# Kernel tuning notes

Hardware: AMD Instinct MI355X
Metric: run time of the kernel (lower is better)

The kernel has to match this reference:

```python
import jax, jax.numpy as jnp
import numpy as np

D = 256; H = 4; DK = D // H
MAX_ATOMS = 13; EDGE_NUM = 78; PAD = 799; K = 20
PREFIX = MAX_ATOMS * 2 + 2 + EDGE_NUM * 4   # 340, tokens that get positional encoding
SEQ = PREFIX + K                             # 360
NPAIR = EDGE_NUM + MAX_ATOMS                 # 91 atom pairs (i,j), j up to max_atoms
DFF = 2048; MSP = 800; B = 256

# ---- static pair / gather index tables (numpy, computed once) ----
def _pairs():
    pi, pj, pe = [], [], []
    for i in range(MAX_ATOMS):
        base = sum(MAX_ATOMS - jj - 1 for jj in range(i))  # getEdgeIdx prefix
        for j in range(i + 1, MAX_ATOMS + 1):
            pi.append(i); pj.append(j); pe.append(base + (j - i) - 1)
    return np.array(pi), np.array(pj), np.array(pe)

PI, PJ, PEI = _pairs()
_eb = MAX_ATOMS * 2 + 2 + 2 * PEI           # edge feature start in encoder output (stride 2)
GIDX = np.stack([2*PI, 2*PI+1, 2*PJ, 2*PJ+1, _eb, _eb+1, _eb+2, _eb+3], axis=1)  # (91,8)
ZMASK = np.ones((NPAIR, 8), np.float32)
ZMASK[PJ == MAX_ATOMS, 4:] = 0.0            # j == max_atoms -> edge slots zeroed
ES = (MAX_ATOMS + 1) * 2 + 4 * PEI          # edge slice start in raw src (stride 4)
EIDX = ES[:, None] + np.arange(4)[None, :]  # (91,4)

def _pe_table():
    pe = np.zeros((PREFIX, D), np.float32)
    pos = np.arange(PREFIX, dtype=np.float64)[:, None]
    ev = np.arange(0, D, 2)
    pe[:, ev] = np.sin(pos / 10000.0 ** (2 * ev / D))
    pe[:, ev + 1] = np.cos(pos / 10000.0 ** (2 * (ev + 1) / D))
    return jnp.asarray(pe)

PETAB = _pe_table()

def _norm(x, a, b):
    mu = x.mean(-1, keepdims=True)
    sd = x.std(-1, keepdims=True, ddof=1)   # torch std is unbiased
    return a * (x - mu) / (sd + 1e-6) + b

def _out_mask(src):
    # vectorized get_pad_mask10; later conditions override earlier ones
    ai = src[:, 2*PI + 1]; aj = src[:, 2*PJ + 1]
    ti = src[:, 2*PI];     tj = src[:, 2*PJ]
    c1 = (ai == 2) | (aj == 2)                                  # -> [0,0,1]
    c2 = (tj == 1) | (ai == 1) | (aj == 1)                      # -> [0,1,1]
    c3 = (ti == PAD) | (tj == PAD) | (ai == 0) | (aj == 0)      # -> [1,1,1]
    c4 = jnp.asarray(PJ < MAX_ATOMS)[None, :] & jnp.any(src[:, EIDX] == 1, axis=-1)
    m111 = c3 | c4
    return jnp.stack([m111, m111 | c2, m111 | c2 | c1], axis=-1)  # (B,91,3) bool


def setup_inputs() -> dict:
    key = jax.random.key(0)
    ks = jax.random.split(key, 12)
    g = lambda k, shape, s=0.02: jax.random.normal(k, shape, jnp.float32) * s
    emb = g(ks[0], (MSP, D), 1.0).at[PAD].set(0.0)  # nn.Embedding zeroes padding row
    return {
        'src': jax.random.randint(ks[1], (B, SEQ), 0, MSP, dtype=jnp.int32),
        'emb': emb,
        'wq': g(ks[2], (D, D)), 'bq': jnp.zeros((D,), jnp.float32),
        'wk': g(ks[3], (D, D)), 'bk': jnp.zeros((D,), jnp.float32),
        'wv': g(ks[4], (D, D)), 'bv': jnp.zeros((D,), jnp.float32),
        'wo': g(ks[5], (D, D)), 'bo': jnp.zeros((D,), jnp.float32),
        'n1a': jnp.ones((D,), jnp.float32), 'n1b': jnp.zeros((D,), jnp.float32),
        'n2a': jnp.ones((D,), jnp.float32), 'n2b': jnp.zeros((D,), jnp.float32),
        'w1': g(ks[6], (D, DFF)), 'b1': jnp.zeros((DFF,), jnp.float32),
        'w2': g(ks[7], (DFF, D)), 'b2': jnp.zeros((D,), jnp.float32),
        'wl': g(ks[8], (8 * D, 3)), 'bl': jnp.zeros((3,), jnp.float32),
    }


def reference(src, emb, wq, bq, wk, bk, wv, bv, wo, bo, n1a, n1b, n2a, n2b,
              w1, b1, w2, b2, wl, bl):
    Bn, S = src.shape
    x = emb[src]                                             # (B,S,D)
    # positional encoding (scale + PE) only on first PREFIX tokens, dropout=eval/no-op
    xp = x[:, :PREFIX] * jnp.sqrt(jnp.float32(D)) + PETAB
    x = jnp.concatenate([xp, x[:, PREFIX:]], axis=1)
    pad = src != PAD                                         # (B,S) query-row mask
    # encoder layer (pre-norm, residual)
    x2 = _norm(x, n1a, n1b)
    def heads(w, b):
        return (x2 @ w + b).reshape(Bn, S, H, DK).transpose(0, 2, 1, 3)
    q, kk, v = heads(wq, bq), heads(wk, bk), heads(wv, bv)
    sc = jnp.einsum('bhqd,bhkd->bhqk', q, kk) / jnp.sqrt(jnp.float32(DK))
    sc = jnp.where(pad[:, None, :, None], sc, jnp.float32(-1e9))  # mask broadcasts over keys
    ctx = jnp.einsum('bhqk,bhkd->bhqd', jax.nn.softmax(sc, axis=-1), v)
    x = x + ctx.transpose(0, 2, 1, 3).reshape(Bn, S, D) @ wo + bo
    x2 = _norm(x, n2a, n2b)
    x = x + jax.nn.relu(x2 @ w1 + b1) @ w2 + b2
    # triangular atom-pair gather + concat, vectorized via static index table
    feat = x[:, GIDX] * jnp.asarray(ZMASK)[None, :, :, None]  # (B,91,8,D)
    logits = feat.reshape(Bn, NPAIR, 8 * D) @ wl + bl         # (B,91,3)
    return jnp.where(_out_mask(src), jnp.float32(-1e9), logits)
```

## Files before the change

### kernel.cpp

```cpp
#include <hip/hip_runtime.h>
#include <hip/hip_bf16.h>
#include <math.h>


using bf16 = __hip_bfloat16;
typedef __attribute__((ext_vector_type(4))) float f32x4;
typedef __attribute__((ext_vector_type(16))) float f32x16;
typedef long long i64;
typedef unsigned char uchar;

static __device__ __forceinline__ float wave_sum64(float v){
  #pragma unroll
  for (int o = 32; o >= 1; o >>= 1) v += __shfl_xor(v, o, 64);
  return v;
}

static __device__ __forceinline__ void gl_lds16(const void* g, void* l){
  __builtin_amdgcn_global_load_lds((const __attribute__((address_space(1))) void*)g,
                                   (__attribute__((address_space(3))) void*)l, 16, 0, 0);
}

static __device__ __forceinline__ void barrier_lgkm(){
  asm volatile("s_waitcnt lgkmcnt(0)" ::: "memory");
  __builtin_amdgcn_s_barrier();
}

static __device__ __forceinline__ unsigned pack2(float a, float b){
  union { bf16 h[2]; unsigned u; } u;
  u.h[0] = __float2bfloat16(a); u.h[1] = __float2bfloat16(b);
  return u.u;
}

static __device__ __forceinline__ uchar f2f8(float v){
  return (uchar)(__builtin_amdgcn_cvt_pk_fp8_f32(v, 0.f, 0, false) & 0xff);
}
static __device__ __forceinline__ unsigned pack4_fp8(float a, float b, float c, float d){
  int v = __builtin_amdgcn_cvt_pk_fp8_f32(a, b, 0, false);
  v = __builtin_amdgcn_cvt_pk_fp8_f32(c, d, v, true);
  return (unsigned)v;
}

static __device__ __forceinline__ float fexp2(float x){
  float r;
  asm("v_exp_f32 %0, %1" : "=v"(r) : "v"(x));
  return r;
}

__global__ __launch_bounds__(256) void cvt_all(
    const float* s0, const float* s1, const float* s2, const float* s3,
    const float* s4, const float* s5,
    uchar* d0, uchar* d1, uchar* d2, uchar* d3, uchar* d4, uchar* d5)
{
  __shared__ float t[32][33];
  const float* srcs[6] = {s0, s1, s2, s3, s4, s5};
  uchar* dsts[6] = {d0, d1, d2, d3, d4, d5};
  const int Ks[6] = {256, 256, 256, 256, 256, 2048};
  const int Ns[6] = {256, 256, 256, 256, 2048, 256};
  const int offs[7] = {0, 64, 128, 192, 256, 768, 1280};
  int bid = blockIdx.x, j = 5;
  #pragma unroll
  for (int q = 4; q >= 0; q--) if (bid < offs[q + 1]) j = q;
  int local = bid - offs[j];
  int K = Ks[j], N = Ns[j];
  const float* src = srcs[j];
  uchar* dst = dsts[j];
  int kt = K >> 5;
  int kb = (local % kt) * 32, nb = (local / kt) * 32;
  int tx = threadIdx.x & 31, ty = threadIdx.x >> 5;
  #pragma unroll
  for (int dy = 0; dy < 32; dy += 8)
    t[ty + dy][tx] = src[(size_t)(kb + ty + dy) * N + nb + tx];
  __syncthreads();
  #pragma unroll
  for (int dy = 0; dy < 32; dy += 8)
    dst[(size_t)(nb + ty + dy) * K + kb + tx] = f2f8(t[tx][ty + dy]);
}

__global__ __launch_bounds__(256) void embed_ln1(
    const int* __restrict__ src, const float* __restrict__ emb,
    const float* __restrict__ na, const float* __restrict__ nb,
    bf16* __restrict__ x, uchar* __restrict__ xn8)
{
  int row  = blockIdx.x * 4 + (threadIdx.x >> 6);
  int lane = threadIdx.x & 63;
  int s = row % 360;
  int tok = src[row];
  float4 v = *(const float4*)(emb + (size_t)tok * 256 + lane * 4);
  float vv[4] = {v.x, v.y, v.z, v.w};
  if (s < 340){
    const float C = (-2.0f / 256.0f) * 13.287712379549449f;
    #pragma unroll
    for (int t = 0; t < 4; t++){
      int c = lane * 4 + t;
      float ang = (float)s * exp2f(C * (float)c);
      float pe = (c & 1) ? cosf(ang) : sinf(ang);
      vv[t] = 16.0f * vv[t] + pe;
    }
  }
  float sum = wave_sum64(vv[0] + vv[1] + vv[2] + vv[3]);
  float mu = sum * (1.0f / 256.0f);
  float d0 = vv[0]-mu, d1 = vv[1]-mu, d2 = vv[2]-mu, d3 = vv[3]-mu;
  float sq = wave_sum64(d0*d0 + d1*d1 + d2*d2 + d3*d3);
  float inv = 1.0f / (sqrtf(sq * (1.0f / 255.0f)) + 1e-6f);
  bf16 xo[4] = { __float2bfloat16(vv[0]), __float2bfloat16(vv[1]),
                 __float2bfloat16(vv[2]), __float2bfloat16(vv[3]) };
  *(uint2*)(x + (size_t)row * 256 + lane * 4) = *(uint2*)xo;
  float4 a4 = *(const float4*)(na + lane * 4);
  float4 b4 = *(const float4*)(nb + lane * 4);
  unsigned u = pack4_fp8(a4.x * d0 * inv + b4.x, a4.y * d1 * inv + b4.y,
                         a4.z * d2 * inv + b4.z, a4.w * d3 * inv + b4.w);
  *(unsigned*)(xn8 + (size_t)row * 256 + lane * 4) = u;
}

__global__ __launch_bounds__(256) void ln_k8(
    const bf16* __restrict__ x, const float* __restrict__ na,
    const float* __restrict__ nb, uchar* __restrict__ xn8)
{
  int row  = blockIdx.x * 4 + (threadIdx.x >> 6);
  int lane = threadIdx.x & 63;
  uint2 raw = *(const uint2*)(x + (size_t)row * 256 + lane * 4);
  bf16* xr = (bf16*)&raw;
  float v0 = __bfloat162float(xr[0]), v1 = __bfloat162float(xr[1]);
  float v2 = __bfloat162float(xr[2]), v3 = __bfloat162float(xr[3]);
  float sum = wave_sum64(v0 + v1 + v2 + v3);
  float mu = sum * (1.0f / 256.0f);
  float d0 = v0-mu, d1 = v1-mu, d2 = v2-mu, d3 = v3-mu;
  float sq = wave_sum64(d0*d0 + d1*d1 + d2*d2 + d3*d3);
  float inv = 1.0f / (sqrtf(sq * (1.0f / 255.0f)) + 1e-6f);
  float4 a4 = *(const float4*)(na + lane * 4);
  float4 b4 = *(const float4*)(nb + lane * 4);
  unsigned u = pack4_fp8(a4.x * d0 * inv + b4.x, a4.y * d1 * inv + b4.y,
                         a4.z * d2 * inv + b4.z, a4.w * d3 * inv + b4.w);
  *(unsigned*)(xn8 + (size_t)row * 256 + lane * 4) = u;
}

template<int MODE>
__global__ __launch_bounds__(256) void gemm_k256(
    const uchar* __restrict__ A, const uchar* __restrict__ Bt,
    const float* __restrict__ bias,
    uchar* __restrict__ out8, bf16* __restrict__ xres,
    int N, int nTiles,
    const float* __restrict__ bq, const float* __restrict__ bk)
{
  __shared__ __align__(16) char smem[65536];
  uchar* As = (uchar*)smem;
  uchar* Bs = (uchar*)(smem + 32768);
  uchar* S8 = (uchar*)smem;
  bf16 (*Cs)[136] = (bf16 (*)[136])smem;
  int chunk = gridDim.x >> 3;
  int bi = (blockIdx.x & 7) * chunk + (blockIdx.x >> 3);
  int m0 = (bi / nTiles) * 128, n0 = (bi % nTiles) * 128;
  int tid = threadIdx.x;
  int wave = tid >> 6, lane = tid & 63;
  int wm = (wave >> 1) * 64, wn = (wave & 1) * 64;
  int r32 = lane & 31, half = lane >> 5;

  #pragma unroll
  for (int j = 0; j < 8; j++){
    int c = j * 256 + tid;
    int row = c >> 4, p = c & 15;
    int sl = (p & 8) | ((p & 7) ^ (row & 7));
    gl_lds16(A  + (size_t)(m0 + row) * 256 + sl * 16, As + (size_t)c * 16);
    gl_lds16(Bt + (size_t)(n0 + row) * 256 + sl * 16, Bs + (size_t)c * 16);
  }

  f32x16 acc[2][2];
  #pragma unroll
  for (int mb = 0; mb < 2; mb++)
    #pragma unroll
    for (int nb = 0; nb < 2; nb++)
      #pragma unroll
      for (int e = 0; e < 16; e++) acc[mb][nb][e] = 0.f;

  __syncthreads();

  #pragma unroll
  for (int c = 0; c < 8; c++){
    int l0 = 2 * c + half;
    i64 alo[2], ahi[2], blo[2], bhi[2];
    #pragma unroll
    for (int mb = 0; mb < 2; mb++){
      int row = wm + mb * 32 + r32;
      int st = (l0 & 8) | ((l0 & 7) ^ (row & 7));
      uint4 v = *(const uint4*)(As + row * 256 + st * 16);
      alo[mb] = *(const i64*)&v.x;  ahi[mb] = *(const i64*)&v.z;
    }
    #pragma unroll
    for (int nb = 0; nb < 2; nb++){
      int row = wn + nb * 32 + r32;
      int st = (l0 & 8) | ((l0 & 7) ^ (row & 7));
      uint4 v = *(const uint4*)(Bs + row * 256 + st * 16);
      blo[nb] = *(const i64*)&v.x;  bhi[nb] = *(const i64*)&v.z;
    }
    #pragma unroll
    for (int mb = 0; mb < 2; mb++)
      #pragma unroll
      for (int nb = 0; nb < 2; nb++){
        if (MODE == 5){
          acc[mb][nb] = __builtin_amdgcn_mfma_f32_32x32x16_fp8_fp8(alo[mb], blo[nb], acc[mb][nb], 0, 0, 0);
          acc[mb][nb] = __builtin_amdgcn_mfma_f32_32x32x16_fp8_fp8(ahi[mb], bhi[nb], acc[mb][nb], 0, 0, 0);
        } else {
          acc[mb][nb] = __builtin_amdgcn_mfma_f32_32x32x16_fp8_fp8(blo[nb], alo[mb], acc[mb][nb], 0, 0, 0);
          acc[mb][nb] = __builtin_amdgcn_mfma_f32_32x32x16_fp8_fp8(bhi[nb], ahi[mb], acc[mb][nb], 0, 0, 0);
        }
      }
  }

  __syncthreads();

  if (MODE == 4){
    const int region = n0 >> 8;
    const float* bb = (region == 0 ? bq : bk);
    #pragma unroll
    for (int mb = 0; mb < 2; mb++){
      int m_l = wm + mb * 32 + r32;
      #pragma unroll
      for (int nb = 0; nb < 2; nb++)
        #pragma unroll
        for (int g = 0; g < 4; g++){
          int n_l = wn + nb * 32 + g * 8 + half * 4;
          int bidx = (n0 & 255) + n_l;
          float v0 = acc[mb][nb][g * 4 + 0] + bb[bidx + 0];
          float v1 = acc[mb][nb][g * 4 + 1] + bb[bidx + 1];
          float v2 = acc[mb][nb][g * 4 + 2] + bb[bidx + 2];
          float v3 = acc[mb][nb][g * 4 + 3] + bb[bidx + 3];
          *(unsigned*)(S8 + m_l * 136 + n_l) = pack4_fp8(v0, v1, v2, v3);
        }
    }
    __syncthreads();
    int lr = tid >> 1, seg = tid & 1;
    #pragma unroll
    for (int j = 0; j < 4; j++){
      int nl = seg * 64 + j * 16;
      uint2 a = *(uint2*)(S8 + lr * 136 + nl);
      uint2 b = *(uint2*)(S8 + lr * 136 + nl + 8);
      uint4 st = make_uint4(a.x, a.y, b.x, b.y);
      int m = m0 + lr;
      int b_ = m / 360, s = m - b_ * 360;
      int nnl = (n0 & 255) + nl;
      int h = nnl >> 6, dk = nnl & 63;
      size_t roff = (region == 1) ? 23592960ull : 0ull;
      *(uint4*)(out8 + roff + ((size_t)(b_ * 4 + h) * 360 + s) * 64 + dk) = st;
    }
  } else if (MODE == 5){
    #pragma unroll
    for (int nb = 0; nb < 2; nb++){
      int n_l = wn + nb * 32 + r32;
      float bv_ = bias[n0 + n_l];
      #pragma unroll
      for (int mb = 0; mb < 2; mb++)
        #pragma unroll
        for (int g = 0; g < 4; g++){
          int m_l = wm + mb * 32 + g * 8 + half * 4;
          *(unsigned*)(S8 + n_l * 136 + m_l) =
              pack4_fp8(acc[mb][nb][g * 4 + 0] + bv_, acc[mb][nb][g * 4 + 1] + bv_,
                        acc[mb][nb][g * 4 + 2] + bv_, acc[mb][nb][g * 4 + 3] + bv_);
        }
    }
    __syncthreads();
    int nn = tid >> 1, part = tid & 1;
    int nnl = n0 + nn;
    int h = nnl >> 6, dk = nnl & 63;
    #pragma unroll
    for (int j0 = 0; j0 < 64; j0 += 8){
      int mm = m0 + part * 64 + j0;
      int b_ = mm / 360, s = mm - b_ * 360;
      uint2 val = *(uint2*)(S8 + nn * 136 + part * 64 + j0);
      *(uint2*)(out8 + ((size_t)((b_ * 4 + h) * 64 + dk)) * 360 + s) = val;
    }
  } else {
    #pragma unroll
    for (int hb = 0; hb < 2; hb++){
      if ((wave >> 1) == hb){
        #pragma unroll
        for (int mb = 0; mb < 2; mb++){
          int ml = mb * 32 + r32;
          #pragma unroll
          for (int nb = 0; nb < 2; nb++)
            #pragma unroll
            for (int g = 0; g < 4; g++){
              int nl0 = wn + nb * 32 + g * 8 + half * 4;
              float v0 = acc[mb][nb][g * 4 + 0] + bias[n0 + nl0 + 0];
              float v1 = acc[mb][nb][g * 4 + 1] + bias[n0 + nl0 + 1];
              float v2 = acc[mb][nb][g * 4 + 2] + bias[n0 + nl0 + 2];
              float v3 = acc[mb][nb][g * 4 + 3] + bias[n0 + nl0 + 3];
              *(unsigned*)(&Cs[ml][nl0])     = pack2(v0, v1);
              *(unsigned*)(&Cs[ml][nl0 + 2]) = pack2(v2, v3);
            }
        }
      }
      __syncthreads();
      int mbase = m0 + hb * 64;
      int lr = tid >> 2, seg = tid & 3;
      bf16* op = xres + (size_t)(mbase + lr) * 256 + n0 + seg * 32;
      #pragma unroll
      for (int j = 0; j < 4; j++){
        uint4 cv = *(uint4*)(&Cs[lr][seg * 32 + j * 8]);
        uint4 xv = *(uint4*)(op + j * 8);
        bf16* ca = (bf16*)&cv; bf16* xa = (bf16*)&xv;
        bf16 o8[8];
        #pragma unroll
        for (int t = 0; t < 8; t++)
          o8[t] = __float2bfloat16(__bfloat162float(ca[t]) + __bfloat162float(xa[t]));
        *(uint4*)(op + j * 8) = *(uint4*)o8;
      }
      __syncthreads();
    }
  }
}

__global__ __launch_bounds__(512) void gemm_ffn(
    const uchar* __restrict__ A, const uchar* __restrict__ W1t,
    const uchar* __restrict__ W2t, const float* __restrict__ b1,
    const float* __restrict__ b2, bf16* __restrict__ xres)
{
  extern __shared__ __align__(16) char sm[];
  const int W1OFF = 32768, W2OFF = 98304;
  int bi = (blockIdx.x & 7) * 90 + (blockIdx.x >> 3);
  int m0 = bi * 128;
  int tid = threadIdx.x;
  int wave = tid >> 6, lane = tid & 63;
  int wm = (wave & 1) * 64, wn = (wave >> 1) * 64;
  int wnh = (wave >> 1) * 32;
  int r32 = lane & 31, half = lane >> 5;

  #pragma unroll
  for (int j = 0; j < 4; j++){
    int c = j * 512 + tid;
    int row = c >> 4, p = c & 15;
    int sl = (p & 8) | ((p & 7) ^ (row & 7));
    gl_lds16(A + (size_t)(m0 + row) * 256 + sl * 16, sm + c * 16);
  }
  #pragma unroll
  for (int j = 0; j < 4; j++){
    int c = j * 512 + tid;
    int row1 = c >> 4, p1 = c & 15;
    int sl1 = (p1 & 8) | ((p1 & 7) ^ (row1 & 7));
    gl_lds16(W1t + (size_t)row1 * 256 + sl1 * 16, sm + W1OFF + c * 16);
    int row2 = c >> 3, p2 = c & 7;
    int sl2 = p2 ^ (row2 & 7);
    gl_lds16(W2t + (size_t)row2 * 2048 + sl2 * 16, sm + W2OFF + c * 16);
  }

  f32x16 acc2[2][2];
  #pragma unroll
  for (int mb = 0; mb < 2; mb++)
    #pragma unroll
    for (int nb = 0; nb < 2; nb++)
      #pragma unroll
      for (int e = 0; e < 16; e++) acc2[mb][nb][e] = 0.f;

  __syncthreads();

  i64 Alo[2][8], Ahi[2][8];
  #pragma unroll
  for (int c = 0; c < 8; c++){
    int l0 = 2 * c + half;
    #pragma unroll
    for (int mb = 0; mb < 2; mb++){
      int row = wm + mb * 32 + r32;
      int st = (l0 & 8) | ((l0 & 7) ^ (row & 7));
      uint4 v = *(const uint4*)(sm + row * 256 + st * 16);
      Alo[mb][c] = *(const i64*)&v.x;  Ahi[mb][c] = *(const i64*)&v.z;
    }
  }

  int cur = 0;
  for (int s = 0; s < 16; s++){
    const int w1o = W1OFF + cur * 32768;
    const int w2o = W2OFF + cur * 32768;

    f32x16 acc1[2];
    #pragma unroll
    for (int mb = 0; mb < 2; mb++)
      #pragma unroll
      for (int e = 0; e < 16; e++) acc1[mb][e] = 0.f;
    #pragma unroll
    for (int c = 0; c < 8; c++){
      int l0 = 2 * c + half;
      int roww = wnh + r32;
      int stw = (l0 & 8) | ((l0 & 7) ^ (roww & 7));
      uint4 w = *(const uint4*)(sm + w1o + roww * 256 + stw * 16);
      i64 wlo = *(const i64*)&w.x, whi = *(const i64*)&w.z;
      #pragma unroll
      for (int mb = 0; mb < 2; mb++){
        acc1[mb] = __builtin_amdgcn_mfma_f32_32x32x16_fp8_fp8(wlo, Alo[mb][c], acc1[mb], 0, 0, 0);
        acc1[mb] = __builtin_amdgcn_mfma_f32_32x32x16_fp8_fp8(whi, Ahi[mb][c], acc1[mb], 0, 0, 0);
      }
    }
    barrier_lgkm();

    if (s < 15){
      int nxt = cur ^ 1;
      #pragma unroll
      for (int j = 0; j < 4; j++){
        int c = j * 512 + tid;
        int row1 = c >> 4, p1 = c & 15;
        int sl1 = (p1 & 8) | ((p1 & 7) ^ (row1 & 7));
        gl_lds16(W1t + (size_t)((s + 1) * 128 + row1) * 256 + sl1 * 16,
                 sm + W1OFF + nxt * 32768 + c * 16);
        int row2 = c >> 3, p2 = c & 7;
        int sl2 = p2 ^ (row2 & 7);
        gl_lds16(W2t + (size_t)row2 * 2048 + (s + 1) * 128 + sl2 * 16,
                 sm + W2OFF + nxt * 32768 + c * 16);
      }
    }

    #pragma unroll
    for (int mb = 0; mb < 2; mb++){
      int m = wm + mb * 32 + r32;
      #pragma unroll
      for (int g = 0; g < 4; g++){
        int n_l = wnh + g * 8 + half * 4;
        float4 bv = *(const float4*)(b1 + s * 128 + n_l);
        float v0 = fmaxf(acc1[mb][g * 4 + 0] + bv.x, 0.f);
        float v1 = fmaxf(acc1[mb][g * 4 + 1] + bv.y, 0.f);
        float v2 = fmaxf(acc1[mb][g * 4 + 2] + bv.z, 0.f);
        float v3 = fmaxf(acc1[mb][g * 4 + 3] + bv.w, 0.f);
        int sl = (n_l >> 4) ^ (m & 7);
        *(unsigned*)(sm + w1o + m * 128 + sl * 16 + (n_l & 15)) =
            pack4_fp8(v0, v1, v2, v3);
      }
    }
    barrier_lgkm();

    #pragma unroll
    for (int c = 0; c < 4; c++){
      int l0 = 2 * c + half;
      i64 hlo[2], hhi[2], wlo[2], whi[2];
      #pragma unroll
      for (int mb = 0; mb < 2; mb++){
        int row = wm + mb * 32 + r32;
        int st = l0 ^ (row & 7);
        uint4 v = *(const uint4*)(sm + w1o + row * 128 + st * 16);
        hlo[mb] = *(const i64*)&v.x;  hhi[mb] = *(const i64*)&v.z;
      }
      #pragma unroll
      for (int nb = 0; nb < 2; nb++){
        int row = wn + nb * 32 + r32;
        int st = l0 ^ (row & 7);
        uint4 v = *(const uint4*)(sm + w2o + row * 128 + st * 16);
        wlo[nb] = *(const i64*)&v.x;  whi[nb] = *(const i64*)&v.z;
      }
      #pragma unroll
      for (int mb = 0; mb < 2; mb++)
        #pragma unroll
        for (int nb = 0; nb < 2; nb++){
          acc2[mb][nb] = __builtin_amdgcn_mfma_f32_32x32x16_fp8_fp8(wlo[nb], hlo[mb], acc2[mb][nb], 0, 0, 0);
          acc2[mb][nb] = __builtin_amdgcn_mfma_f32_32x32x16_fp8_fp8(whi[nb], hhi[mb], acc2[mb][nb], 0, 0, 0);
        }
    }
    __syncthreads();
    cur ^= 1;
  }

  bf16 (*Cs)[264] = (bf16 (*)[264])(sm + W1OFF);
  #pragma unroll
  for (int mb = 0; mb < 2; mb++){
    int ml = wm + mb * 32 + r32;
    #pragma unroll
    for (int nb = 0; nb < 2; nb++)
      #pragma unroll
      for (int g = 0; g < 4; g++){
        int nl0 = wn + nb * 32 + g * 8 + half * 4;
        float4 bv = *(const float4*)(b2 + nl0);
        float v0 = acc2[mb][nb][g * 4 + 0] + bv.x;
        float v1 = acc2[mb][nb][g * 4 + 1] + bv.y;
        float v2 = acc2[mb][nb][g * 4 + 2] + bv.z;
        float v3 = acc2[mb][nb][g * 4 + 3] + bv.w;
        *(unsigned*)(&Cs[ml][nl0])     = pack2(v0, v1);
        *(unsigned*)(&Cs[ml][nl0 + 2]) = pack2(v2, v3);
      }
  }
  __syncthreads();
  int lr = tid >> 2, seg = tid & 3;
  bf16* op = xres + (size_t)(m0 + lr) * 256 + seg * 64;
  #pragma unroll
  for (int j = 0; j < 8; j++){
    uint4 cv = *(uint4*)(&Cs[lr][seg * 64 + j * 8]);
    uint4 xv = *(uint4*)(op + j * 8);
    bf16* ca = (bf16*)&cv; bf16* xa = (bf16*)&xv;
    bf16 o8[8];
    #pragma unroll
    for (int t = 0; t < 8; t++)
      o8[t] = __float2bfloat16(__bfloat162float(ca[t]) + __bfloat162float(xa[t]));
    *(uint4*)(op + j * 8) = *(uint4*)o8;
  }
}

template<bool TAIL>
static __device__ __forceinline__ void attn_step(
    int kc, const uchar (*Ks)[80], uchar (*Pb)[16][48],
    const uchar* __restrict__ vb, int wave, int r, int qd,
    const i64* qa0, const i64* qa1, float* lsum, f32x4 (*accO)[4])
{
  int krow0 = kc * 32 + r;
  int krow1 = krow0 + 16;
  if (TAIL){ if (krow0 > 359) krow0 = 359; if (krow1 > 359) krow1 = 359; }
  i64 kf00 = *(const i64*)(&Ks[krow0][qd * 8]);
  i64 kf01 = *(const i64*)(&Ks[krow0][32 + qd * 8]);
  i64 kf10 = *(const i64*)(&Ks[krow1][qd * 8]);
  i64 kf11 = *(const i64*)(&Ks[krow1][32 + qd * 8]);
  i64 vf[4];
  #pragma unroll
  for (int dt = 0; dt < 4; dt++)
    vf[dt] = *(const i64*)(vb + (size_t)(dt * 16 + r) * 360 + kc * 32 + qd * 8);

  const float CEXP = 0.18033688011112042f;

  #pragma unroll
  for (int tl = 0; tl < 3; tl++){
    f32x4 z0 = {0.f, 0.f, 0.f, 0.f}, z1 = {0.f, 0.f, 0.f, 0.f};
    z0 = __builtin_amdgcn_mfma_f32_16x16x32_fp8_fp8(kf00, qa0[tl], z0, 0, 0, 0);
    z0 = __builtin_amdgcn_mfma_f32_16x16x32_fp8_fp8(kf01, qa1[tl], z0, 0, 0, 0);
    z1 = __builtin_amdgcn_mfma_f32_16x16x32_fp8_fp8(kf10, qa0[tl], z1, 0, 0, 0);
    z1 = __builtin_amdgcn_mfma_f32_16x16x32_fp8_fp8(kf11, qa1[tl], z1, 0, 0, 0);
    float p0[4], p1[4];
    #pragma unroll
    for (int i = 0; i < 4; i++){
      p0[i] = fexp2(z0[i] * CEXP);
      p1[i] = fexp2(z1[i] * CEXP);
      if (TAIL){
        if (kc * 32 + qd * 4 + i >= 360) p0[i] = 0.f;
        if (kc * 32 + 16 + qd * 4 + i >= 360) p1[i] = 0.f;
      }
      lsum[tl] += p0[i] + p1[i];
    }
    *(unsigned*)(&Pb[wave][r][qd * 4])      = pack4_fp8(p0[0], p0[1], p0[2], p0[3]);
    *(unsigned*)(&Pb[wave][r][16 + qd * 4]) = pack4_fp8(p1[0], p1[1], p1[2], p1[3]);
    asm volatile("s_waitcnt lgkmcnt(0)" ::: "memory");
    i64 pa = *(const i64*)(&Pb[wave][r][qd * 8]);
    #pragma unroll
    for (int dt = 0; dt < 4; dt++)
      accO[tl][dt] = __builtin_amdgcn_mfma_f32_16x16x32_fp8_fp8(pa, vf[dt], accO[tl][dt], 0, 0, 0);
    asm volatile("s_waitcnt lgkmcnt(0)" ::: "memory");
  }
}

__global__ __launch_bounds__(512) void attn5(
    const uchar* __restrict__ q, const uchar* __restrict__ kk, const uchar* __restrict__ vt,
    const int* __restrict__ src, uchar* __restrict__ ctx8)
{
  __shared__ __align__(16) uchar smem[34944];
  uchar (*Ks)[80]     = (uchar (*)[80])smem;
  uchar (*Pb)[16][48] = (uchar (*)[16][48])(smem + 28800);
  int bh = blockIdx.x;
  int b = bh >> 2, h = bh & 3;
  int wave = threadIdx.x >> 6, lane = threadIdx.x & 63;
  int r = lane & 15, qd = lane >> 4;
  const uchar* qb = q  + (size_t)bh * 360 * 64;
  const uchar* kb = kk + (size_t)bh * 360 * 64;
  const uchar* vb = vt + (size_t)bh * 64 * 360;
  const int* srow = src + b * 360;

  for (int c = threadIdx.x; c < 1440; c += 512){
    int row = c >> 2, g = c & 3;
    *(uint4*)(&Ks[row][g * 16]) = *(const uint4*)(kb + row * 64 + g * 16);
  }
  __syncthreads();

  i64 qa0[3], qa1[3];
  float lsum[3];
  f32x4 accO[3][4];
  #pragma unroll
  for (int tl = 0; tl < 3; tl++){
    int qt = wave * 3 + tl;
    int qg = qt * 16 + r;
    int qrow = qg > 359 ? 359 : qg;
    bool qp = (qg < 360) && (srow[qg] == 799);
    i64 a0 = *(const i64*)(qb + qrow * 64 + qd * 8);
    i64 a1 = *(const i64*)(qb + qrow * 64 + 32 + qd * 8);
    qa0[tl] = qp ? 0 : a0;
    qa1[tl] = qp ? 0 : a1;
    lsum[tl] = 0.f;
    #pragma unroll
    for (int dt = 0; dt < 4; dt++) accO[tl][dt] = (f32x4){0.f, 0.f, 0.f, 0.f};
  }

  for (int kc = 0; kc < 11; kc++)
    attn_step<false>(kc, Ks, Pb, vb, wave, r, qd, qa0, qa1, lsum, accO);
  attn_step<true>(11, Ks, Pb, vb, wave, r, qd, qa0, qa1, lsum, accO);

  __syncthreads();
  uchar* Cw = smem + wave * 1280;

  #pragma unroll
  for (int tl = 0; tl < 3; tl++){
    float ls = lsum[tl];
    ls += __shfl_xor(ls, 16, 64);
    ls += __shfl_xor(ls, 32, 64);
    float invl = 1.0f / ls;
    #pragma unroll
    for (int dt = 0; dt < 4; dt++)
      *(unsigned*)(Cw + r * 80 + dt * 16 + qd * 4) =
          pack4_fp8(accO[tl][dt][0] * invl, accO[tl][dt][1] * invl,
                    accO[tl][dt][2] * invl, accO[tl][dt][3] * invl);
    asm volatile("s_waitcnt lgkmcnt(0)" ::: "memory");
    int qt = wave * 3 + tl;
    int qglob = qt * 16 + r;
    if (qglob < 360)
      *(uint4*)(ctx8 + ((size_t)(b * 360 + qglob)) * 256 + h * 64 + qd * 16) =
          *(uint4*)(Cw + r * 80 + qd * 16);
    asm volatile("s_waitcnt lgkmcnt(0)" ::: "memory");
  }
}

__global__ __launch_bounds__(256) void head_k(
    const bf16* __restrict__ x, const int* __restrict__ src,
    const float* __restrict__ wl, const float* __restrict__ bl,
    float* __restrict__ out)
{
  __shared__ bf16 Xs[192][264];
  int b = blockIdx.x;
  int tid = threadIdx.x;
  int wave = tid >> 6, lane = tid & 63;
  int g = lane >> 3, sub = lane & 7;

  const bf16* xb = x + (size_t)b * 360 * 256;
  for (int it = 0; it < 24; it++){
    int idx = tid + it * 256;
    int row = idx >> 5, col = idx & 31;
    *(uint4*)(&Xs[row][col * 8]) = *(const uint4*)(xb + row * 256 + col * 8);
  }

  float wv[96];
  {
    const float4* wr4 = (const float4*)(wl + (size_t)(g * 256 + sub * 32) * 3);
    #pragma unroll
    for (int c = 0; c < 24; c++) *(float4*)(&wv[c * 4]) = wr4[c];
  }
  float bl0 = bl[0], bl1 = bl[1], bl2 = bl[2];
  const int* sr = src + b * 360;
  __syncthreads();

  for (int p = wave; p < 91; p += 4){
    int i = 0, rem = p;
    while (rem >= 13 - i){ rem -= 13 - i; i++; }
    int j = i + 1 + rem;
    int base = 12 * i - (i * (i - 1)) / 2;
    int pe = base + (j - i) - 1;
    int eb = 28 + 2 * pe;

    int idxg;
    if (g == 0) idxg = 2 * i;
    else if (g == 1) idxg = 2 * i + 1;
    else if (g == 2) idxg = 2 * j;
    else if (g == 3) idxg = 2 * j + 1;
    else idxg = eb + (g - 4);
    bool zm = !(g >= 4 && j == 13);

    uint4 xv[4];
    #pragma unroll
    for (int c = 0; c < 4; c++) xv[c] = *(uint4*)(&Xs[idxg][sub * 32 + c * 8]);
    const bf16* xa = (const bf16*)xv;
    float a0 = 0.f, a1 = 0.f, a2 = 0.f;
    #pragma unroll
    for (int t = 0; t < 32; t++){
      float f = zm ? __bfloat162float(xa[t]) : 0.0f;
      a0 += f * wv[t * 3 + 0];
      a1 += f * wv[t * 3 + 1];
      a2 += f * wv[t * 3 + 2];
    }
    #pragma unroll
    for (int o = 1; o < 64; o <<= 1){
      a0 += __shfl_xor(a0, o, 64);
      a1 += __shfl_xor(a1, o, 64);
      a2 += __shfl_xor(a2, o, 64);
    }
    if (lane == 0){
      int ti = sr[2 * i], ai = sr[2 * i + 1], tj = sr[2 * j], aj = sr[2 * j + 1];
      bool c1 = (ai == 2) || (aj == 2);
      bool c2 = (tj == 1) || (ai == 1) || (aj == 1);
      bool c3 = (ti == 799) || (tj == 799) || (ai == 0) || (aj == 0);
      bool c4 = false;
      if (j < 13){
        int es = 28 + 4 * pe;
        c4 = (sr[es] == 1) || (sr[es + 1] == 1) || (sr[es + 2] == 1) || (sr[es + 3] == 1);
      }
      bool m1 = c3 || c4, m2 = m1 || c2, m3 = m2 || c1;
      float* op = out + ((size_t)b * 91 + p) * 3;
      op[0] = m1 ? -1.0e9f : (a0 + bl0);
      op[1] = m2 ? -1.0e9f : (a1 + bl1);
      op[2] = m3 ? -1.0e9f : (a2 + bl2);
    }
  }
}

extern "C" void kernel_launch(void* const* d_in, const int* in_sizes, int n_in,
                              void* d_out, int out_size, void* d_ws, size_t ws_size,
                              hipStream_t stream)
{
  const int*   src = (const int*)  d_in[0];
  const float* emb = (const float*)d_in[1];
  const float* wq  = (const float*)d_in[2];  const float* bq = (const float*)d_in[3];
  const float* wk  = (const float*)d_in[4];  const float* bk = (const float*)d_in[5];
  const float* wv  = (const float*)d_in[6];  const float* bv = (const float*)d_in[7];
  const float* wo  = (const float*)d_in[8];  const float* bo = (const float*)d_in[9];
  const float* n1a = (const float*)d_in[10]; const float* n1b = (const float*)d_in[11];
  const float* n2a = (const float*)d_in[12]; const float* n2b = (const float*)d_in[13];
  const float* w1  = (const float*)d_in[14]; const float* b1 = (const float*)d_in[15];
  const float* w2  = (const float*)d_in[16]; const float* b2 = (const float*)d_in[17];
  const float* wl  = (const float*)d_in[18]; const float* bl = (const float*)d_in[19];
  float* out = (float*)d_out;

  if (ws_size < 191365120ull) return;

  char* ws = (char*)d_ws;
  bf16*  x    = (bf16*)(ws);
  uchar* xn8  = (uchar*)(ws + 47185920ull);
  char*  R    = ws + 70778880ull;
  uchar* q8   = (uchar*)(R);
  uchar* vt8  = (uchar*)(R + 47185920ull);
  char*  wC   = ws + 165150720ull;
  uchar* wqkv8 = (uchar*)(wC);
  uchar* wo8   = (uchar*)(wC + 196608);
  uchar* w1f8T = (uchar*)(wC + 262144);
  uchar* w2f8T = (uchar*)(wC + 786432);

  cvt_all<<<1280, 256, 0, stream>>>(wq, wk, wv, wo, w1, w2,
                                    wqkv8, wqkv8 + 65536, wqkv8 + 131072,
                                    wo8, w1f8T, w2f8T);

  embed_ln1<<<23040, 256, 0, stream>>>(src, emb, n1a, n1b, x, xn8);

  gemm_k256<4><<<2880, 256, 0, stream>>>(xn8, wqkv8, nullptr, q8, nullptr,
                                         512, 4, bq, bk);
  gemm_k256<5><<<1440, 256, 0, stream>>>(xn8, wqkv8 + 131072, bv, vt8, nullptr,
                                         256, 2, nullptr, nullptr);

  attn5<<<1024, 512, 0, stream>>>(q8, q8 + 23592960ull, vt8, src, xn8 );

  gemm_k256<3><<<1440, 256, 0, stream>>>(xn8, wo8, bo, nullptr, x,
                                         256, 2, nullptr, nullptr);

  ln_k8<<<23040, 256, 0, stream>>>(x, n2a, n2b, xn8);

  gemm_ffn<<<720, 512, 163840, stream>>>(xn8, w1f8T, w2f8T, b1, b2, x);

  head_k<<<256, 256, 0, stream>>>(x, src, wl, bl, out);
}
```

Measured before the change: 496.9 us.

## Shrink FFN kernel LDS to single buffer to raise occupancy

The fused FFN kernel drops its double-buffered W1/W2 tiles. A single 64 KB region is now reused for the A tile, the W1/W2 slices and the hidden activations, and launch bounds request 4 waves per SIMD. Next-slice weight loads are issued only after the second GEMM finishes, with a barrier, so global-load latency is no longer overlapped with compute inside a block. The intent is that more resident blocks per CU hide that latency instead. The epilogue is split into two half-tile passes so the output staging fits the smaller buffer.

```diff
diff --git a/kernel.cpp b/kernel.cpp
--- a/kernel.cpp
+++ b/kernel.cpp
@@ -309,13 +309,13 @@
   }
 }
 
-__global__ __launch_bounds__(512) void gemm_ffn(
+__global__ __launch_bounds__(512, 4) void gemm_ffn(
     const uchar* __restrict__ A, const uchar* __restrict__ W1t,
     const uchar* __restrict__ W2t, const float* __restrict__ b1,
     const float* __restrict__ b2, bf16* __restrict__ xres)
 {
   extern __shared__ __align__(16) char sm[];
-  const int W1OFF = 32768, W2OFF = 98304;
+  const int W2OFF = 32768;
   int bi = (blockIdx.x & 7) * 90 + (blockIdx.x >> 3);
   int m0 = bi * 128;
   int tid = threadIdx.x;
@@ -331,25 +331,6 @@
     int sl = (p & 8) | ((p & 7) ^ (row & 7));
     gl_lds16(A + (size_t)(m0 + row) * 256 + sl * 16, sm + c * 16);
   }
-  #pragma unroll
-  for (int j = 0; j < 4; j++){
-    int c = j * 512 + tid;
-    int row1 = c >> 4, p1 = c & 15;
-    int sl1 = (p1 & 8) | ((p1 & 7) ^ (row1 & 7));
-    gl_lds16(W1t + (size_t)row1 * 256 + sl1 * 16, sm + W1OFF + c * 16);
-    int row2 = c >> 3, p2 = c & 7;
-    int sl2 = p2 ^ (row2 & 7);
-    gl_lds16(W2t + (size_t)row2 * 2048 + sl2 * 16, sm + W2OFF + c * 16);
-  }
-
-  f32x16 acc2[2][2];
-  #pragma unroll
-  for (int mb = 0; mb < 2; mb++)
-    #pragma unroll
-    for (int nb = 0; nb < 2; nb++)
-      #pragma unroll
-      for (int e = 0; e < 16; e++) acc2[mb][nb][e] = 0.f;
-
   __syncthreads();
 
   i64 Alo[2][8], Ahi[2][8];
@@ -364,12 +345,30 @@
       Alo[mb][c] = *(const i64*)&v.x;  Ahi[mb][c] = *(const i64*)&v.z;
     }
   }
-
-  int cur = 0;
+  barrier_lgkm();
+
+  #pragma unroll
+  for (int j = 0; j < 4; j++){
+    int c = j * 512 + tid;
+    int row1 = c >> 4, p1 = c & 15;
+    int sl1 = (p1 & 8) | ((p1 & 7) ^ (row1 & 7));
+    gl_lds16(W1t + (size_t)row1 * 256 + sl1 * 16, sm + c * 16);
+    int row2 = c >> 3, p2 = c & 7;
+    int sl2 = p2 ^ (row2 & 7);
+    gl_lds16(W2t + (size_t)row2 * 2048 + sl2 * 16, sm + W2OFF + c * 16);
+  }
+
+  f32x16 acc2[2][2];
+  #pragma unroll
+  for (int mb = 0; mb < 2; mb++)
+    #pragma unroll
+    for (int nb = 0; nb < 2; nb++)
+      #pragma unroll
+      for (int e = 0; e < 16; e++) acc2[mb][nb][e] = 0.f;
+
+  __syncthreads();
+
   for (int s = 0; s < 16; s++){
-    const int w1o = W1OFF + cur * 32768;
-    const int w2o = W2OFF + cur * 32768;
-
     f32x16 acc1[2];
     #pragma unroll
     for (int mb = 0; mb < 2; mb++)
@@ -380,7 +379,7 @@
       int l0 = 2 * c + half;
       int roww = wnh + r32;
       int stw = (l0 & 8) | ((l0 & 7) ^ (roww & 7));
-      uint4 w = *(const uint4*)(sm + w1o + roww * 256 + stw * 16);
+      uint4 w = *(const uint4*)(sm + roww * 256 + stw * 16);
       i64 wlo = *(const i64*)&w.x, whi = *(const i64*)&w.z;
       #pragma unroll
       for (int mb = 0; mb < 2; mb++){
@@ -389,22 +388,6 @@
       }
     }
     barrier_lgkm();
-
-    if (s < 15){
-      int nxt = cur ^ 1;
-      #pragma unroll
-      for (int j = 0; j < 4; j++){
-        int c = j * 512 + tid;
-        int row1 = c >> 4, p1 = c & 15;
-        int sl1 = (p1 & 8) | ((p1 & 7) ^ (row1 & 7));
-        gl_lds16(W1t + (size_t)((s + 1) * 128 + row1) * 256 + sl1 * 16,
-                 sm + W1OFF + nxt * 32768 + c * 16);
-        int row2 = c >> 3, p2 = c & 7;
-        int sl2 = p2 ^ (row2 & 7);
-        gl_lds16(W2t + (size_t)row2 * 2048 + (s + 1) * 128 + sl2 * 16,
-                 sm + W2OFF + nxt * 32768 + c * 16);
-      }
-    }
 
     #pragma unroll
     for (int mb = 0; mb < 2; mb++){
@@ -418,7 +401,7 @@
         float v2 = fmaxf(acc1[mb][g * 4 + 2] + bv.z, 0.f);
         float v3 = fmaxf(acc1[mb][g * 4 + 3] + bv.w, 0.f);
         int sl = (n_l >> 4) ^ (m & 7);
-        *(unsigned*)(sm + w1o + m * 128 + sl * 16 + (n_l & 15)) =
+        *(unsigned*)(sm + m * 128 + sl * 16 + (n_l & 15)) =
             pack4_fp8(v0, v1, v2, v3);
       }
     }
@@ -432,14 +415,14 @@
       for (int mb = 0; mb < 2; mb++){
         int row = wm + mb * 32 + r32;
         int st = l0 ^ (row & 7);
-        uint4 v = *(const uint4*)(sm + w1o + row * 128 + st * 16);
+        uint4 v = *(const uint4*)(sm + row * 128 + st * 16);
         hlo[mb] = *(const i64*)&v.x;  hhi[mb] = *(const i64*)&v.z;
       }
       #pragma unroll
       for (int nb = 0; nb < 2; nb++){
         int row = wn + nb * 32 + r32;
         int st = l0 ^ (row & 7);
-        uint4 v = *(const uint4*)(sm + w2o + row * 128 + st * 16);
+        uint4 v = *(const uint4*)(sm + W2OFF + row * 128 + st * 16);
         wlo[nb] = *(const i64*)&v.x;  whi[nb] = *(const i64*)&v.z;
       }
       #pragma unroll
@@ -450,41 +433,62 @@
           acc2[mb][nb] = __builtin_amdgcn_mfma_f32_32x32x16_fp8_fp8(whi[nb], hhi[mb], acc2[mb][nb], 0, 0, 0);
         }
     }
+    barrier_lgkm();
+
+    if (s < 15){
+      #pragma unroll
+      for (int j = 0; j < 4; j++){
+        int c = j * 512 + tid;
+        int row1 = c >> 4, p1 = c & 15;
+        int sl1 = (p1 & 8) | ((p1 & 7) ^ (row1 & 7));
+        gl_lds16(W1t + (size_t)((s + 1) * 128 + row1) * 256 + sl1 * 16,
+                 sm + c * 16);
+        int row2 = c >> 3, p2 = c & 7;
+        int sl2 = p2 ^ (row2 & 7);
+        gl_lds16(W2t + (size_t)row2 * 2048 + (s + 1) * 128 + sl2 * 16,
+                 sm + W2OFF + c * 16);
+      }
+      __syncthreads();
+    }
+  }
+
+  bf16 (*Cs)[264] = (bf16 (*)[264])sm;
+  #pragma unroll
+  for (int hb = 0; hb < 2; hb++){
+    if ((wave & 1) == hb){
+      #pragma unroll
+      for (int mb = 0; mb < 2; mb++){
+        int ml = mb * 32 + r32;
+        #pragma unroll
+        for (int nb = 0; nb < 2; nb++)
+          #pragma unroll
+          for (int g = 0; g < 4; g++){
+            int nl0 = wn + nb * 32 + g * 8 + half * 4;
+            float4 bv = *(const float4*)(b2 + nl0);
+            float v0 = acc2[mb][nb][g * 4 + 0] + bv.x;
+            float v1 = acc2[mb][nb][g * 4 + 1] + bv.y;
+            float v2 = acc2[mb][nb][g * 4 + 2] + bv.z;
+            float v3 = acc2[mb][nb][g * 4 + 3] + bv.w;
+            *(unsigned*)(&Cs[ml][nl0])     = pack2(v0, v1);
+            *(unsigned*)(&Cs[ml][nl0 + 2]) = pack2(v2, v3);
+          }
+      }
+    }
     __syncthreads();
-    cur ^= 1;
-  }
-
-  bf16 (*Cs)[264] = (bf16 (*)[264])(sm + W1OFF);
-  #pragma unroll
-  for (int mb = 0; mb < 2; mb++){
-    int ml = wm + mb * 32 + r32;
-    #pragma unroll
-    for (int nb = 0; nb < 2; nb++)
-      #pragma unroll
-      for (int g = 0; g < 4; g++){
-        int nl0 = wn + nb * 32 + g * 8 + half * 4;
-        float4 bv = *(const float4*)(b2 + nl0);
-        float v0 = acc2[mb][nb][g * 4 + 0] + bv.x;
-        float v1 = acc2[mb][nb][g * 4 + 1] + bv.y;
-        float v2 = acc2[mb][nb][g * 4 + 2] + bv.z;
-        float v3 = acc2[mb][nb][g * 4 + 3] + bv.w;
-        *(unsigned*)(&Cs[ml][nl0])     = pack2(v0, v1);
-        *(unsigned*)(&Cs[ml][nl0 + 2]) = pack2(v2, v3);
-      }
-  }
-  __syncthreads();
-  int lr = tid >> 2, seg = tid & 3;
-  bf16* op = xres + (size_t)(m0 + lr) * 256 + seg * 64;
-  #pragma unroll
-  for (int j = 0; j < 8; j++){
-    uint4 cv = *(uint4*)(&Cs[lr][seg * 64 + j * 8]);
-    uint4 xv = *(uint4*)(op + j * 8);
-    bf16* ca = (bf16*)&cv; bf16* xa = (bf16*)&xv;
-    bf16 o8[8];
-    #pragma unroll
-    for (int t = 0; t < 8; t++)
-      o8[t] = __float2bfloat16(__bfloat162float(ca[t]) + __bfloat162float(xa[t]));
-    *(uint4*)(op + j * 8) = *(uint4*)o8;
+    int lr = tid >> 3, seg = tid & 7;
+    bf16* op = xres + (size_t)(m0 + hb * 64 + lr) * 256 + seg * 32;
+    #pragma unroll
+    for (int j = 0; j < 4; j++){
+      uint4 cv = *(uint4*)(&Cs[lr][seg * 32 + j * 8]);
+      uint4 xv = *(uint4*)(op + j * 8);
+      bf16* ca = (bf16*)&cv; bf16* xa = (bf16*)&xv;
+      bf16 o8[8];
+      #pragma unroll
+      for (int t = 0; t < 8; t++)
+        o8[t] = __float2bfloat16(__bfloat162float(ca[t]) + __bfloat162float(xa[t]));
+      *(uint4*)(op + j * 8) = *(uint4*)o8;
+    }
+    __syncthreads();
   }
 }
 
@@ -735,7 +739,7 @@
 
   ln_k8<<<23040, 256, 0, stream>>>(x, n2a, n2b, xn8);
 
-  gemm_ffn<<<720, 512, 163840, stream>>>(xn8, w1f8T, w2f8T, b1, b2, x);
+  gemm_ffn<<<720, 512, 65536, stream>>>(xn8, w1f8T, w2f8T, b1, b2, x);
 
   head_k<<<256, 256, 0, stream>>>(x, src, wl, bl, out);
 }
```

After: 792.3 us. 1.59x slower.
